# Performance work log

Measured on AMD Instinct MI355X. Metric: run time of the kernel, lower is better.

Reference implementation:

```python
import jax, jax.numpy as jnp
import numpy as np

B, S, E, H, W, HID, V, OUT, L = 2, 2048, 512, 8, 5, 2048, 32000, 6, 6
DH = E // H
SCALE = DH ** -0.5
PAD = (W - 1) // 2
SK = S - W + 1  # number of k/v windows from torch unfold


def setup_inputs() -> dict:
    key = jax.random.key(0)
    ks = jax.random.split(key, 16)
    def g(i, shape, s):
        return jax.random.normal(ks[i], shape, jnp.float32) * s
    return {
        "inputs": jax.random.randint(ks[0], (B, S), 0, V),
        "emb": g(1, (V, E), 0.02),
        "ln_w": jnp.ones((E,), jnp.float32),
        "ln_b": jnp.zeros((E,), jnp.float32),
        "q_w": g(2, (E, E), E ** -0.5), "q_b": jnp.zeros((E,), jnp.float32),
        "k_w": g(3, (E, E), E ** -0.5), "k_b": jnp.zeros((E,), jnp.float32),
        "v_w": g(4, (E, E), E ** -0.5), "v_b": jnp.zeros((E,), jnp.float32),
        "fc1_w": g(5, (E, HID), E ** -0.5), "fc1_b": jnp.zeros((HID,), jnp.float32),
        "fc2_w": g(6, (HID, E), HID ** -0.5), "fc2_b": jnp.zeros((E,), jnp.float32),
        "out_w": g(7, (E * S, OUT), (E * S) ** -0.5), "out_b": jnp.zeros((OUT,), jnp.float32),
    }


def _pos_encoding():
    pos = jnp.arange(S, dtype=jnp.float32)[:, None]
    div = jnp.exp(jnp.arange(0, E, 2, dtype=jnp.float32) * (-np.log(10000.0) / E))
    pe = jnp.zeros((S, E), jnp.float32)
    pe = pe.at[:, 0::2].set(jnp.sin(pos * div)).at[:, 1::2].set(jnp.cos(pos * div))
    return pe


def reference(inputs, emb, ln_w, ln_b, q_w, q_b, k_w, k_b, v_w, v_b,
              fc1_w, fc1_b, fc2_w, fc2_b, out_w, out_b):
    x = emb[inputs] + _pos_encoding()  # [B,S,E]

    def ln(t):
        m = t.mean(-1, keepdims=True)
        v_ = t.var(-1, keepdims=True)
        return (t - m) / jnp.sqrt(v_ + 1e-5) * ln_w + ln_b

    def attn(x):
        def heads(w, b):
            return (x @ w + b).reshape(B, S, H, DH).transpose(0, 2, 1, 3)  # [B,H,S,dh]
        q, k, v = heads(q_w, q_b), heads(k_w, k_b), heads(v_w, v_b)
        qp = jnp.pad(q, ((0, 0), (0, 0), (PAD, PAD), (0, 0)))  # [B,H,S+W-1,dh]
        # torch unfold -> windows [..., dh, W]; einsum contracts dh AND W, so flatten both.
        q_un = jnp.stack([qp[:, :, j:j + S, :] for j in range(W)], axis=-1).reshape(B, H, S, DH * W)
        k_un = jnp.stack([k[:, :, j:j + SK, :] for j in range(W)], axis=-1).reshape(B, H, SK, DH * W)
        scores = jnp.einsum('bhqf,bhkf->bhqk', q_un, k_un) * SCALE  # [B,H,S,SK]
        a = jax.nn.softmax(scores, axis=-1)
        # output einsum 'bnqk,bnkdh->bnqd' sums attn-weighted v over k AND window dim;
        # since attn is independent of window pos, presum v over the window.
        v_sum = sum(v[:, :, j:j + SK, :] for j in range(W))  # [B,H,SK,dh]
        o = jnp.einsum('bhqk,bhkd->bhqd', a, v_sum)
        return o.transpose(0, 2, 1, 3).reshape(B, S, E)

    for _ in range(L):
        x = ln(attn(x))
        x = (jax.nn.relu(x @ fc1_w + fc1_b) @ fc2_w + fc2_b) + x
        x = ln(x)
    return x.reshape(B, -1) @ out_w + out_b  # [B,OUT]
```

## Files before the change

### kernel.cpp

```cpp
#include <hip/hip_runtime.h>
#include <math.h>


namespace {
constexpr int kB   = 2;
constexpr int kS   = 2048;
constexpr int kE   = 512;
constexpr int kH   = 8;
constexpr int kDH  = 64;
constexpr int kSK  = 2044;
constexpr int kHID = 2048;
constexpr int kL   = 6;
constexpr float kScaleL2 = 0.125f * 1.44269504088896f;
constexpr int kTok = kB * kS;
constexpr int kNX  = kTok * kE;
constexpr int kQKV = 3 * kE;
constexpr int kSQ  = 72;
constexpr int kSV  = 136;
}

using f16x8   = __attribute__((ext_vector_type(8))) _Float16;
using floatx4 = __attribute__((ext_vector_type(4))) float;

static __device__ __forceinline__ unsigned short f2h(float f) {
  return __builtin_bit_cast(unsigned short, (_Float16)f);
}
static __device__ __forceinline__ float h2f(unsigned short u) {
  return (float)__builtin_bit_cast(_Float16, u);
}
static __device__ __forceinline__ unsigned int pk2h(float a, float b) {
  return __builtin_bit_cast(unsigned int, __builtin_amdgcn_cvt_pkrtz(a, b));
}

__global__ __launch_bounds__(256) void embed_kernel(const int* __restrict__ idx,
        const float* __restrict__ emb, unsigned short* __restrict__ X) {
  const int bs  = blockIdx.x;
  const int s   = bs & (kS - 1);
  const int tok = idx[bs];
  const int t   = threadIdx.x;
#pragma unroll
  for (int r = 0; r < 2; ++r) {
    const int e = t + 256 * r;
    const int i = e >> 1;
    const float dv  = __expf((float)(2 * i) * (-9.210340371976184f / (float)kE));
    const float ang = (float)s * dv;
    const float pe  = (e & 1) ? cosf(ang) : sinf(ang);
    X[bs * kE + e] = f2h(emb[tok * kE + e] + pe);
  }
}

__global__ __launch_bounds__(256) void tcast_kernel(const float* __restrict__ src,
        unsigned short* __restrict__ dst, int K, int N) {
  __shared__ float t[32][33];
  const int tid = threadIdx.x;
  const int tx = tid & 31, ty = tid >> 5;
  const int n0 = blockIdx.x * 32, k0 = blockIdx.y * 32;
#pragma unroll
  for (int p = 0; p < 4; ++p)
    t[ty + 8 * p][tx] = src[(size_t)(k0 + ty + 8 * p) * N + n0 + tx];
  __syncthreads();
#pragma unroll
  for (int p = 0; p < 4; ++p)
    dst[(size_t)(n0 + ty + 8 * p) * K + k0 + tx] = f2h(t[tx][ty + 8 * p]);
}

__global__ __launch_bounds__(256) void qkvb_kernel(const float* __restrict__ qb,
        const float* __restrict__ kb, const float* __restrict__ vb,
        float* __restrict__ dst) {
  const int i = blockIdx.x * 256 + threadIdx.x;
  dst[i] = (i < 512) ? qb[i] : ((i < 1024) ? kb[i - 512] : vb[i - 1024]);
}

template <int RELU, int RES>
__global__ __launch_bounds__(256) void mfma_gemm(const unsigned short* __restrict__ A,
        const unsigned short* __restrict__ Bt, const float* __restrict__ bias,
        const unsigned short* __restrict__ Rm, unsigned short* __restrict__ C,
        int M, int N, int K) {
  __shared__ __align__(16) unsigned short As[128 * 40];
  __shared__ __align__(16) unsigned short Bs[128 * 40];
  const int tid = threadIdx.x;
  const int m0 = blockIdx.y * 128, n0 = blockIdx.x * 128;
  const int wid = tid >> 6, lane = tid & 63;
  const int lm = lane & 15, quad = lane >> 4;
  const int wm = (wid & 1) * 64, wn = (wid >> 1) * 64;
  const int bn = tid >> 2, bk = (tid & 3) * 8;
  floatx4 acc[4][4] = {};
  for (int k0 = 0; k0 < K; k0 += 32) {
#pragma unroll
    for (int p = 0; p < 2; ++p) {
      const uint4 va = *(const uint4*)&A[(size_t)(m0 + bn + 64 * p) * K + k0 + bk];
      *(uint4*)&As[(bn + 64 * p) * 40 + bk] = va;
      const uint4 vb = *(const uint4*)&Bt[(size_t)(n0 + bn + 64 * p) * K + k0 + bk];
      *(uint4*)&Bs[(bn + 64 * p) * 40 + bk] = vb;
    }
    __syncthreads();
    f16x8 af[4], bf[4];
#pragma unroll
    for (int t = 0; t < 4; ++t) {
      af[t] = *(const f16x8*)&As[(wm + t * 16 + lm) * 40 + quad * 8];
      bf[t] = *(const f16x8*)&Bs[(wn + t * 16 + lm) * 40 + quad * 8];
    }
#pragma unroll
    for (int mt = 0; mt < 4; ++mt)
#pragma unroll
      for (int nt = 0; nt < 4; ++nt)
        acc[mt][nt] = __builtin_amdgcn_mfma_f32_16x16x32_f16(
            af[mt], bf[nt], acc[mt][nt], 0, 0, 0);
    __syncthreads();
  }
#pragma unroll
  for (int mt = 0; mt < 4; ++mt) {
#pragma unroll
    for (int nt = 0; nt < 4; ++nt) {
      const int n = n0 + wn + nt * 16 + lm;
      const float bv = bias[n];
#pragma unroll
      for (int r = 0; r < 4; ++r) {
        const int m = m0 + wm + mt * 16 + quad * 4 + r;
        float o = acc[mt][nt][r] + bv;
        if (RES) o += h2f(Rm[(size_t)m * N + n]);
        if (RELU) o = fmaxf(o, 0.f);
        C[(size_t)m * N + n] = f2h(o);
      }
    }
  }
}

__global__ __launch_bounds__(256) void vsumt_kernel(const unsigned short* __restrict__ QKVh,
        unsigned short* __restrict__ VsT) {
  const int t0 = blockIdx.x * 64;
  const int h = blockIdx.y, b = blockIdx.z;
  const int tid = threadIdx.x;
  __shared__ float Ls[68 * 65];
  for (int id = tid; id < 68 * 8; id += 256) {
    const int row = id >> 3, d8 = (id & 7) * 8;
    const int gt = t0 + row;
    float v[8];
    if (gt < kS) {
      const unsigned short* p =
          &QKVh[(size_t)(b * kS + gt) * kQKV + 2 * kE + h * kDH + d8];
      const ushort4 a = *(const ushort4*)p;
      const ushort4 c = *(const ushort4*)(p + 4);
      v[0] = h2f(a.x); v[1] = h2f(a.y); v[2] = h2f(a.z); v[3] = h2f(a.w);
      v[4] = h2f(c.x); v[5] = h2f(c.y); v[6] = h2f(c.z); v[7] = h2f(c.w);
    } else {
#pragma unroll
      for (int j = 0; j < 8; ++j) v[j] = 0.f;
    }
#pragma unroll
    for (int j = 0; j < 8; ++j) Ls[row * 65 + d8 + j] = v[j];
  }
  __syncthreads();
  const int t4 = (tid & 15) * 4;
#pragma unroll
  for (int c = 0; c < 4; ++c) {
    const int d = (tid >> 4) + 16 * c;
    ushort4 o;
    unsigned short* op = (unsigned short*)&o;
#pragma unroll
    for (int j = 0; j < 4; ++j) {
      const int tl = t4 + j;
      float s = Ls[(tl + 0) * 65 + d] + Ls[(tl + 1) * 65 + d]
              + Ls[(tl + 2) * 65 + d] + Ls[(tl + 3) * 65 + d]
              + Ls[(tl + 4) * 65 + d];
      if (t0 + tl >= kSK) s = 0.f;
      op[j] = f2h(s);
    }
    *(ushort4*)&VsT[((size_t)(b * kH + h) * kDH + d) * (size_t)kS + t0 + t4] = o;
  }
}

__global__ __launch_bounds__(512) void flash_kernel(const unsigned short* __restrict__ QKVh,
        const unsigned short* __restrict__ VsT, unsigned short* __restrict__ O) {
  const int tid = threadIdx.x;
  const int qt = blockIdx.x, h = blockIdx.y, b = blockIdx.z;
  const int q0 = qt * 64;
  const int wid = tid >> 6, lane = tid & 63;
  const int lm = lane & 15, quad = lane >> 4;
  const int wq = wid >> 2, wt = wid & 3;
  const int bh = b * kH + h;

  __shared__ __align__(16) unsigned short Qs[68 * kSQ];
  __shared__ __align__(16) unsigned short Ks[132 * kSQ];
  __shared__ __align__(16) unsigned short Vt[64 * kSV];
  __shared__ __align__(16) unsigned short Ps[64 * kSV];
  __shared__ float mM[64][4], lM[64][4];

  for (int id = tid; id < 68 * 16; id += 512) {
    const int row = id >> 4, c4 = (id & 15) * 4;
    const int gq = q0 - 2 + row;
    ushort4 v = make_ushort4(0, 0, 0, 0);
    if (gq >= 0 && gq < kS)
      v = *(const ushort4*)&QKVh[(size_t)(b * kS + gq) * kQKV + h * kDH + c4];
    *(ushort4*)&Qs[row * kSQ + c4] = v;
  }

  const int prow = tid >> 4;
  const int pc4 = (tid & 15) * 4, pc8 = (tid & 15) * 8;
  ushort4 kreg[5];
  uint4 vreg[2];
#define PREFETCH(T0)                                                          \
  {                                                                           \
    _Pragma("unroll")                                                         \
    for (int p = 0; p < 5; ++p) {                                             \
      const int row = prow + 32 * p;                                          \
      ushort4 v = make_ushort4(0, 0, 0, 0);                                   \
      if (row < 132) {                                                        \
        const int gk = (T0) + row;                                            \
        if (gk < kS)                                                          \
          v = *(const ushort4*)&QKVh[(size_t)(b * kS + gk) * kQKV + kE +      \
                                     h * kDH + pc4];                          \
      }                                                                       \
      kreg[p] = v;                                                            \
    }                                                                         \
    _Pragma("unroll")                                                         \
    for (int p = 0; p < 2; ++p)                                               \
      vreg[p] = *(const uint4*)&VsT[((size_t)bh * kDH + prow + 32 * p) *      \
                                    (size_t)kS + (T0) + pc8];                 \
  }
  PREFETCH(0)

  float mrow[2], lrow[2];
  mrow[0] = mrow[1] = -1e30f;
  lrow[0] = lrow[1] = 0.f;
  floatx4 Oacc[2][4] = {};
  const int asrc = (lane >> 2) & 12;

  for (int t0 = 0; t0 < kSK; t0 += 128) {
    __syncthreads();
#pragma unroll
    for (int p = 0; p < 5; ++p) {
      const int row = prow + 32 * p;
      if (row < 132) *(ushort4*)&Ks[row * kSQ + pc4] = kreg[p];
    }
#pragma unroll
    for (int p = 0; p < 2; ++p)
      *(uint4*)&Vt[(prow + 32 * p) * kSV + pc8] = vreg[p];
    __syncthreads();
    const int tn = t0 + 128;
    if (tn < kSK) PREFETCH(tn)

    floatx4 sac[2][2] = {};
    __builtin_amdgcn_s_setprio(1);
#pragma unroll
    for (int kk = 0; kk < 10; ++kk) {
      const int w = kk >> 1, d0 = (kk & 1) * 32;
      const f16x8 kf0 = *(const f16x8*)&Ks[(wt * 32 + lm + w) * kSQ + d0 + quad * 8];
      const f16x8 kf1 = *(const f16x8*)&Ks[(wt * 32 + 16 + lm + w) * kSQ + d0 + quad * 8];
      const f16x8 qf0 = *(const f16x8*)&Qs[(wq * 32 + lm + w) * kSQ + d0 + quad * 8];
      const f16x8 qf1 = *(const f16x8*)&Qs[(wq * 32 + 16 + lm + w) * kSQ + d0 + quad * 8];
      sac[0][0] = __builtin_amdgcn_mfma_f32_16x16x32_f16(kf0, qf0, sac[0][0], 0, 0, 0);
      sac[0][1] = __builtin_amdgcn_mfma_f32_16x16x32_f16(kf0, qf1, sac[0][1], 0, 0, 0);
      sac[1][0] = __builtin_amdgcn_mfma_f32_16x16x32_f16(kf1, qf0, sac[1][0], 0, 0, 0);
      sac[1][1] = __builtin_amdgcn_mfma_f32_16x16x32_f16(kf1, qf1, sac[1][1], 0, 0, 0);
    }
    __builtin_amdgcn_s_setprio(0);

    if (t0 + wt * 32 + 32 > kSK) {
#pragma unroll
      for (int tf = 0; tf < 2; ++tf)
#pragma unroll
        for (int r = 0; r < 4; ++r) {
          const int tg = t0 + wt * 32 + tf * 16 + quad * 4 + r;
          if (tg >= kSK) { sac[tf][0][r] = -1e30f; sac[tf][1][r] = -1e30f; }
        }
    }

    float alpha_q[2];
#pragma unroll
    for (int qf = 0; qf < 2; ++qf) {
      float mx = fmaxf(
          fmaxf(fmaxf(sac[0][qf][0], sac[0][qf][1]), fmaxf(sac[0][qf][2], sac[0][qf][3])),
          fmaxf(fmaxf(sac[1][qf][0], sac[1][qf][1]), fmaxf(sac[1][qf][2], sac[1][qf][3])));
      mx = fmaxf(mx, __shfl_xor(mx, 16));
      mx = fmaxf(mx, __shfl_xor(mx, 32));
      const float mnew = fmaxf(mrow[qf], mx * kScaleL2);
      const float al = exp2f(mrow[qf] - mnew);
      float e[2][4];
#pragma unroll
      for (int tf = 0; tf < 2; ++tf)
#pragma unroll
        for (int r = 0; r < 4; ++r)
          e[tf][r] = exp2f(fmaf(sac[tf][qf][r], kScaleL2, -mnew));
      float ps = ((e[0][0] + e[0][1]) + (e[0][2] + e[0][3]))
               + ((e[1][0] + e[1][1]) + (e[1][2] + e[1][3]));
      ps += __shfl_xor(ps, 16);
      ps += __shfl_xor(ps, 32);
      lrow[qf] = lrow[qf] * al + ps;
      mrow[qf] = mnew;
      alpha_q[qf] = al;
      const int rowp = (wq * 32 + qf * 16 + lm) * kSV + wt * 32;
#pragma unroll
      for (int tf = 0; tf < 2; ++tf) {
        *(unsigned int*)&Ps[rowp + tf * 16 + quad * 4]     = pk2h(e[tf][0], e[tf][1]);
        *(unsigned int*)&Ps[rowp + tf * 16 + quad * 4 + 2] = pk2h(e[tf][2], e[tf][3]);
      }
    }
    float alpha_o[2][4];
#pragma unroll
    for (int qf = 0; qf < 2; ++qf)
#pragma unroll
      for (int r = 0; r < 4; ++r)
        alpha_o[qf][r] = __shfl(alpha_q[qf], asrc + r);
    __asm__ volatile("s_waitcnt lgkmcnt(0)" ::: "memory");
#pragma unroll
    for (int ms = 0; ms < 2; ++ms)
#pragma unroll
      for (int nt2 = 0; nt2 < 4; ++nt2)
#pragma unroll
        for (int r = 0; r < 4; ++r)
          Oacc[ms][nt2][r] *= alpha_o[ms][r];
    {
      const int tcol = wt * 32 + quad * 8;
      const f16x8 pf0 = *(const f16x8*)&Ps[(wq * 32 + lm) * kSV + tcol];
      const f16x8 pf1 = *(const f16x8*)&Ps[(wq * 32 + 16 + lm) * kSV + tcol];
      __builtin_amdgcn_s_setprio(1);
#pragma unroll
      for (int nt2 = 0; nt2 < 4; ++nt2) {
        const f16x8 vf = *(const f16x8*)&Vt[(nt2 * 16 + lm) * kSV + tcol];
        Oacc[0][nt2] = __builtin_amdgcn_mfma_f32_16x16x32_f16(pf0, vf, Oacc[0][nt2], 0, 0, 0);
        Oacc[1][nt2] = __builtin_amdgcn_mfma_f32_16x16x32_f16(pf1, vf, Oacc[1][nt2], 0, 0, 0);
      }
      __builtin_amdgcn_s_setprio(0);
    }
  }
  if (quad == 0) {
#pragma unroll
    for (int qf = 0; qf < 2; ++qf) {
      const int row = wq * 32 + qf * 16 + lm;
      mM[row][wt] = mrow[qf];
      lM[row][wt] = lrow[qf];
    }
  }
  __syncthreads();
  float fac[2][4], invL[2][4];
#pragma unroll
  for (int qf = 0; qf < 2; ++qf)
#pragma unroll
    for (int r = 0; r < 4; ++r) {
      const int row = wq * 32 + qf * 16 + quad * 4 + r;
      const float M = fmaxf(fmaxf(mM[row][0], mM[row][1]),
                            fmaxf(mM[row][2], mM[row][3]));
      const float L = lM[row][0] * exp2f(mM[row][0] - M)
                    + lM[row][1] * exp2f(mM[row][1] - M)
                    + lM[row][2] * exp2f(mM[row][2] - M)
                    + lM[row][3] * exp2f(mM[row][3] - M);
      fac[qf][r] = exp2f(mM[row][wt] - M);
      invL[qf][r] = 1.f / L;
    }
  float* OfA = (float*)Vt;
  float* OfB = (float*)Ps;
  if (!(wt & 1)) {
    float* Of = (wt == 0) ? OfA : OfB;
#pragma unroll
    for (int ms = 0; ms < 2; ++ms)
#pragma unroll
      for (int nt2 = 0; nt2 < 4; ++nt2)
#pragma unroll
        for (int r = 0; r < 4; ++r)
          Of[(wq * 32 + ms * 16 + quad * 4 + r) * 68 + nt2 * 16 + lm] =
              Oacc[ms][nt2][r] * fac[ms][r];
  }
  __syncthreads();
  if (wt & 1) {
    float* Of = (wt == 1) ? OfA : OfB;
#pragma unroll
    for (int ms = 0; ms < 2; ++ms)
#pragma unroll
      for (int nt2 = 0; nt2 < 4; ++nt2)
#pragma unroll
        for (int r = 0; r < 4; ++r)
          Of[(wq * 32 + ms * 16 + quad * 4 + r) * 68 + nt2 * 16 + lm] +=
              Oacc[ms][nt2][r] * fac[ms][r];
  }
  __syncthreads();
  if (wt == 0) {
#pragma unroll
    for (int ms = 0; ms < 2; ++ms)
#pragma unroll
      for (int r = 0; r < 4; ++r) {
        const int row = wq * 32 + ms * 16 + quad * 4 + r;
        const int q = q0 + row;
#pragma unroll
        for (int nt2 = 0; nt2 < 4; ++nt2) {
          const float o = (OfA[row * 68 + nt2 * 16 + lm]
                           + OfB[row * 68 + nt2 * 16 + lm]) * invL[ms][r];
          O[(size_t)(b * kS + q) * kE + h * kDH + nt2 * 16 + lm] = f2h(o);
        }
      }
  }
}

__global__ __launch_bounds__(256) void ln_kernel(const unsigned short* __restrict__ Xin,
        const float* __restrict__ w, const float* __restrict__ bb,
        unsigned short* __restrict__ Y) {
  const int row = blockIdx.x;
  const int tid = threadIdx.x;
  const unsigned short* xr = Xin + (size_t)row * kE;
  const ushort2 vv = *(const ushort2*)&xr[tid * 2];
  const float v0 = h2f(vv.x), v1 = h2f(vv.y);
  float s = v0 + v1, sq = v0 * v0 + v1 * v1;
  for (int off = 32; off; off >>= 1) {
    s  += __shfl_down(s, off);
    sq += __shfl_down(sq, off);
  }
  __shared__ float rs[4], rq[4];
  const int wid = tid >> 6;
  if ((tid & 63) == 0) { rs[wid] = s; rq[wid] = sq; }
  __syncthreads();
  const float St = rs[0] + rs[1] + rs[2] + rs[3];
  const float Qt = rq[0] + rq[1] + rq[2] + rq[3];
  const float mean = St * (1.f / kE);
  const float var  = Qt * (1.f / kE) - mean * mean;
  const float rstd = rsqrtf(var + 1e-5f);
  const float2 wv = *(const float2*)&w[tid * 2];
  const float2 bv = *(const float2*)&bb[tid * 2];
  ushort2 o;
  o.x = f2h((v0 - mean) * rstd * wv.x + bv.x);
  o.y = f2h((v1 - mean) * rstd * wv.y + bv.y);
  *(ushort2*)&(Y + (size_t)row * kE)[tid * 2] = o;
}

__global__ __launch_bounds__(256) void final_kernel(const unsigned short* __restrict__ X,
        const float* __restrict__ Wt, const float* __restrict__ bias,
        float* __restrict__ out) {
  const int b = blockIdx.y, chunk = blockIdx.x;
  const int tid = threadIdx.x;
  const unsigned short* xb = X + (size_t)b * (kS * kE);
  float acc[6] = {};
  const int k0 = chunk * 8192;
#pragma unroll 4
  for (int i = 0; i < 32; ++i) {
    const int kk = k0 + tid + i * 256;
    const float xv = h2f(xb[kk]);
    const float* wr = Wt + (size_t)kk * 6;
#pragma unroll
    for (int o = 0; o < 6; ++o) acc[o] = fmaf(xv, wr[o], acc[o]);
  }
#pragma unroll
  for (int o = 0; o < 6; ++o)
    for (int off = 32; off; off >>= 1) acc[o] += __shfl_down(acc[o], off);
  __shared__ float part[4][6];
  const int wid = tid >> 6;
  if ((tid & 63) == 0) {
#pragma unroll
    for (int o = 0; o < 6; ++o) part[wid][o] = acc[o];
  }
  __syncthreads();
  if (tid < 6) {
    float s2 = part[0][tid] + part[1][tid] + part[2][tid] + part[3][tid];
    if (chunk == 0) s2 += bias[tid];
    atomicAdd(&out[b * 6 + tid], s2);
  }
}

extern "C" void kernel_launch(void* const* d_in, const int* in_sizes, int n_in,
                              void* d_out, int out_size, void* d_ws, size_t ws_size,
                              hipStream_t stream) {
  (void)in_sizes; (void)n_in; (void)ws_size;
  const int*   tok   = (const int*)d_in[0];
  const float* emb   = (const float*)d_in[1];
  const float* ln_w  = (const float*)d_in[2];
  const float* ln_b  = (const float*)d_in[3];
  const float* q_w   = (const float*)d_in[4];
  const float* q_b   = (const float*)d_in[5];
  const float* k_w   = (const float*)d_in[6];
  const float* k_b   = (const float*)d_in[7];
  const float* v_w   = (const float*)d_in[8];
  const float* v_b   = (const float*)d_in[9];
  const float* fc1_w = (const float*)d_in[10];
  const float* fc1_b = (const float*)d_in[11];
  const float* fc2_w = (const float*)d_in[12];
  const float* fc2_b = (const float*)d_in[13];
  const float* out_w = (const float*)d_in[14];
  const float* out_b = (const float*)d_in[15];

  float* ws = (float*)d_ws;
  unsigned short* x16 = (unsigned short*)ws;
  unsigned short* y16 = (unsigned short*)(ws + (size_t)kNX / 2);
  float* regA = ws + (size_t)kNX;
  unsigned short* qkvh = (unsigned short*)regA;
  unsigned short* hbuf = (unsigned short*)regA;
  unsigned short* wqkvT = (unsigned short*)(ws + (size_t)3 * kNX);
  unsigned short* fc1T  = wqkvT + (size_t)kQKV * kE;
  unsigned short* fc2T  = fc1T + (size_t)kHID * kE;
  float* qkvb = (float*)(fc2T + (size_t)kE * kHID);
  unsigned short* vsT = (unsigned short*)(qkvb + kQKV);

  tcast_kernel<<<dim3(16, 16), 256, 0, stream>>>(q_w, wqkvT, kE, kE);
  tcast_kernel<<<dim3(16, 16), 256, 0, stream>>>(k_w, wqkvT + (size_t)kE * kE, kE, kE);
  tcast_kernel<<<dim3(16, 16), 256, 0, stream>>>(v_w, wqkvT + (size_t)2 * kE * kE, kE, kE);
  tcast_kernel<<<dim3(64, 16), 256, 0, stream>>>(fc1_w, fc1T, kE, kHID);
  tcast_kernel<<<dim3(16, 64), 256, 0, stream>>>(fc2_w, fc2T, kHID, kE);
  qkvb_kernel<<<dim3(6), 256, 0, stream>>>(q_b, k_b, v_b, qkvb);

  embed_kernel<<<dim3(kTok), 256, 0, stream>>>(tok, emb, x16);
  for (int l = 0; l < kL; ++l) {
    mfma_gemm<0, 0><<<dim3(kQKV / 128, kTok / 128), 256, 0, stream>>>(
        x16, wqkvT, qkvb, nullptr, qkvh, kTok, kQKV, kE);
    vsumt_kernel<<<dim3(kS / 64, kH, kB), 256, 0, stream>>>(qkvh, vsT);
    flash_kernel<<<dim3(kS / 64, kH, kB), 512, 0, stream>>>(qkvh, vsT, y16);
    ln_kernel<<<dim3(kTok), 256, 0, stream>>>(y16, ln_w, ln_b, x16);
    mfma_gemm<1, 0><<<dim3(kHID / 128, kTok / 128), 256, 0, stream>>>(
        x16, fc1T, fc1_b, nullptr, hbuf, kTok, kHID, kE);
    mfma_gemm<0, 1><<<dim3(kE / 128, kTok / 128), 256, 0, stream>>>(
        hbuf, fc2T, fc2_b, x16, y16, kTok, kE, kHID);
    ln_kernel<<<dim3(kTok), 256, 0, stream>>>(y16, ln_w, ln_b, x16);
  }
  hipMemsetAsync(d_out, 0, (size_t)out_size * sizeof(float), stream);
  final_kernel<<<dim3(128, kB), 256, 0, stream>>>(x16, out_w, out_b, (float*)d_out);
}
```

Before: 1.263 ms.

## Build P fragments in registers via permlane swaps instead of LDS round-trip

In the flash attention kernel, the softmax probabilities are no longer written to a shared-memory Ps buffer and read back as MFMA A-operands. They are repacked in registers using permlane32/permlane16 swaps to form the f16x8 fragments directly. The row max/sum cross-lane reductions also switch from shfl_xor (LDS-routed bpermute) to permlane swaps. This removes LDS traffic and a wait, and frees the Ps allocation, so the epilogue reuses Ks as scratch. The risk is wrong fragment ordering and reliance on a gfx950-specific permlane swap builtin.

Result: no change. 1.249 ms (-1.1%).

```diff
diff --git a/kernel.cpp b/kernel.cpp
--- a/kernel.cpp
+++ b/kernel.cpp
@@ -21,6 +21,8 @@
 
 using f16x8   = __attribute__((ext_vector_type(8))) _Float16;
 using floatx4 = __attribute__((ext_vector_type(4))) float;
+using uint2v  = __attribute__((ext_vector_type(2))) unsigned int;
+using uint4v  = __attribute__((ext_vector_type(4))) unsigned int;
 
 static __device__ __forceinline__ unsigned short f2h(float f) {
   return __builtin_bit_cast(unsigned short, (_Float16)f);
@@ -30,6 +32,16 @@
 }
 static __device__ __forceinline__ unsigned int pk2h(float a, float b) {
   return __builtin_bit_cast(unsigned int, __builtin_amdgcn_cvt_pkrtz(a, b));
+}
+static __device__ __forceinline__ float red16(float x, bool hi) {
+  const unsigned u = __builtin_bit_cast(unsigned, x);
+  const uint2v r = __builtin_amdgcn_permlane16_swap(u, u, false, false);
+  return __builtin_bit_cast(float, hi ? r[0] : r[1]);
+}
+static __device__ __forceinline__ float red32(float x, bool hi) {
+  const unsigned u = __builtin_bit_cast(unsigned, x);
+  const uint2v r = __builtin_amdgcn_permlane32_swap(u, u, false, false);
+  return __builtin_bit_cast(float, hi ? r[0] : r[1]);
 }
 
 __global__ __launch_bounds__(256) void embed_kernel(const int* __restrict__ idx,
@@ -177,13 +189,13 @@
   const int q0 = qt * 64;
   const int wid = tid >> 6, lane = tid & 63;
   const int lm = lane & 15, quad = lane >> 4;
+  const bool h16 = (lane & 16) != 0, h32 = (lane & 32) != 0;
   const int wq = wid >> 2, wt = wid & 3;
   const int bh = b * kH + h;
 
   __shared__ __align__(16) unsigned short Qs[68 * kSQ];
   __shared__ __align__(16) unsigned short Ks[132 * kSQ];
   __shared__ __align__(16) unsigned short Vt[64 * kSV];
-  __shared__ __align__(16) unsigned short Ps[64 * kSV];
   __shared__ float mM[64][4], lM[64][4];
 
   for (int id = tid; id < 68 * 16; id += 512) {
@@ -267,13 +279,14 @@
     }
 
     float alpha_q[2];
+    f16x8 pfrag[2];
 #pragma unroll
     for (int qf = 0; qf < 2; ++qf) {
       float mx = fmaxf(
           fmaxf(fmaxf(sac[0][qf][0], sac[0][qf][1]), fmaxf(sac[0][qf][2], sac[0][qf][3])),
           fmaxf(fmaxf(sac[1][qf][0], sac[1][qf][1]), fmaxf(sac[1][qf][2], sac[1][qf][3])));
-      mx = fmaxf(mx, __shfl_xor(mx, 16));
-      mx = fmaxf(mx, __shfl_xor(mx, 32));
+      mx = fmaxf(mx, red16(mx, h16));
+      mx = fmaxf(mx, red32(mx, h32));
       const float mnew = fmaxf(mrow[qf], mx * kScaleL2);
       const float al = exp2f(mrow[qf] - mnew);
       float e[2][4];
@@ -284,17 +297,22 @@
           e[tf][r] = exp2f(fmaf(sac[tf][qf][r], kScaleL2, -mnew));
       float ps = ((e[0][0] + e[0][1]) + (e[0][2] + e[0][3]))
                + ((e[1][0] + e[1][1]) + (e[1][2] + e[1][3]));
-      ps += __shfl_xor(ps, 16);
-      ps += __shfl_xor(ps, 32);
+      ps += red16(ps, h16);
+      ps += red32(ps, h32);
       lrow[qf] = lrow[qf] * al + ps;
       mrow[qf] = mnew;
       alpha_q[qf] = al;
-      const int rowp = (wq * 32 + qf * 16 + lm) * kSV + wt * 32;
-#pragma unroll
-      for (int tf = 0; tf < 2; ++tf) {
-        *(unsigned int*)&Ps[rowp + tf * 16 + quad * 4]     = pk2h(e[tf][0], e[tf][1]);
-        *(unsigned int*)&Ps[rowp + tf * 16 + quad * 4 + 2] = pk2h(e[tf][2], e[tf][3]);
-      }
+      const unsigned w00 = pk2h(e[0][0], e[0][1]);
+      const unsigned w01 = pk2h(e[0][2], e[0][3]);
+      const unsigned w10 = pk2h(e[1][0], e[1][1]);
+      const unsigned w11 = pk2h(e[1][2], e[1][3]);
+      const uint2v sA = __builtin_amdgcn_permlane32_swap(w00, w10, false, false);
+      const uint2v dA = __builtin_amdgcn_permlane16_swap(sA[0], sA[1], false, false);
+      const uint2v sB = __builtin_amdgcn_permlane32_swap(w01, w11, false, false);
+      const uint2v dB = __builtin_amdgcn_permlane16_swap(sB[0], sB[1], false, false);
+      uint4v fr;
+      fr[0] = dA[0]; fr[1] = dB[0]; fr[2] = dA[1]; fr[3] = dB[1];
+      pfrag[qf] = __builtin_bit_cast(f16x8, fr);
     }
     float alpha_o[2][4];
 #pragma unroll
@@ -302,7 +320,6 @@
 #pragma unroll
       for (int r = 0; r < 4; ++r)
         alpha_o[qf][r] = __shfl(alpha_q[qf], asrc + r);
-    __asm__ volatile("s_waitcnt lgkmcnt(0)" ::: "memory");
 #pragma unroll
     for (int ms = 0; ms < 2; ++ms)
 #pragma unroll
@@ -312,14 +329,12 @@
           Oacc[ms][nt2][r] *= alpha_o[ms][r];
     {
       const int tcol = wt * 32 + quad * 8;
-      const f16x8 pf0 = *(const f16x8*)&Ps[(wq * 32 + lm) * kSV + tcol];
-      const f16x8 pf1 = *(const f16x8*)&Ps[(wq * 32 + 16 + lm) * kSV + tcol];
       __builtin_amdgcn_s_setprio(1);
 #pragma unroll
       for (int nt2 = 0; nt2 < 4; ++nt2) {
         const f16x8 vf = *(const f16x8*)&Vt[(nt2 * 16 + lm) * kSV + tcol];
-        Oacc[0][nt2] = __builtin_amdgcn_mfma_f32_16x16x32_f16(pf0, vf, Oacc[0][nt2], 0, 0, 0);
-        Oacc[1][nt2] = __builtin_amdgcn_mfma_f32_16x16x32_f16(pf1, vf, Oacc[1][nt2], 0, 0, 0);
+        Oacc[0][nt2] = __builtin_amdgcn_mfma_f32_16x16x32_f16(pfrag[0], vf, Oacc[0][nt2], 0, 0, 0);
+        Oacc[1][nt2] = __builtin_amdgcn_mfma_f32_16x16x32_f16(pfrag[1], vf, Oacc[1][nt2], 0, 0, 0);
       }
       __builtin_amdgcn_s_setprio(0);
     }
@@ -349,7 +364,7 @@
       invL[qf][r] = 1.f / L;
     }
   float* OfA = (float*)Vt;
-  float* OfB = (float*)Ps;
+  float* OfB = (float*)Ks;
   if (!(wt & 1)) {
     float* Of = (wt == 0) ? OfA : OfB;
 #pragma unroll
```
